# Kernel tuning notes

Hardware: AMD Instinct MI355X
Metric: run time of the kernel (lower is better)

## Reference

```python
import jax, jax.numpy as jnp
import numpy as np

N_E = 8192
DIM = 256
BETA = 0.25


def _l2norm(x, eps=1e-12):
    # matches F.normalize(p=2, dim=-1): x / max(||x||, eps)
    n = jnp.sqrt(jnp.sum(x * x, axis=-1, keepdims=True))
    return x / jnp.maximum(n, eps)


def setup_inputs() -> dict:
    key = jax.random.key(0)
    k1, k2 = jax.random.split(key)
    z = jax.random.normal(k1, (8, 1024, DIM), dtype=jnp.float32)
    embedding_weight = jax.random.normal(k2, (N_E, DIM), dtype=jnp.float32)
    return {"z": z, "embedding_weight": embedding_weight}


def reference(z, embedding_weight):
    z = _l2norm(z)                                   # [B,S,D]
    zf = z.reshape(-1, DIM)                          # [N,D]
    embed_norm = _l2norm(embedding_weight)           # [n_e,D]
    # d = ||z||^2 + ||e||^2 - 2 z.e  -> [N, n_e]
    d = (jnp.sum(zf * zf, axis=1, keepdims=True)
         + jnp.sum(embed_norm * embed_norm, axis=1)
         - 2.0 * jnp.einsum('bd,nd->bn', zf, embed_norm))
    encoding_indices = jnp.argmin(d, axis=1).reshape(z.shape[:-1])  # [B,S]
    z_q = embedding_weight[encoding_indices]          # gather raw codes
    z_q = _l2norm(z_q)                                # [B,S,D]
    loss = (BETA * jnp.mean((jax.lax.stop_gradient(z_q) - z) ** 2)
            + jnp.mean((z_q - jax.lax.stop_gradient(z)) ** 2))
    z_q = z + jax.lax.stop_gradient(z_q - z)          # straight-through
    return z_q, loss, encoding_indices
```

## Files before the change

kernel.cpp:

```cpp
#include <hip/hip_runtime.h>
#include <hip/hip_fp16.h>
#include <cfloat>
#include <math.h>

#define DIM    256
#define N_TOK  8192
#define N_E    8192
#define NSEG   1024
#define MARGIN 0.012f

typedef __attribute__((ext_vector_type(8))) short bf16x8;
typedef __attribute__((ext_vector_type(4))) float f32x4;
typedef __attribute__((ext_vector_type(8))) unsigned short ushort8;

__device__ __forceinline__ unsigned short f2bf(float f) {
    unsigned u = __float_as_uint(f);
    unsigned r = u + 0x7fff + ((u >> 16) & 1);
    return (unsigned short)(r >> 16);
}
__device__ __forceinline__ unsigned fkey(float f) {
    unsigned u = __float_as_uint(f);
    return (u & 0x80000000u) ? ~u : (u | 0x80000000u);
}
__device__ __forceinline__ unsigned short f2h(float f) {
    const __half h = __float2half(f);
    return *(const unsigned short*)&h;
}
__device__ __forceinline__ float h2f(unsigned short u) {
    __half_raw r; r.x = u;
    return __half2float((__half)r);
}

__global__ __launch_bounds__(256) void l2norm_all(const float* __restrict__ z,
                                                  const float* __restrict__ emb,
                                                  float* __restrict__ zn,
                                                  unsigned short* __restrict__ zb,
                                                  float* __restrict__ en,
                                                  unsigned short* __restrict__ esw,
                                                  float* __restrict__ e2) {
    const int lane = threadIdx.x & 63;
    const bool isE = blockIdx.x < (N_E / 4);
    const int row = (isE ? blockIdx.x : blockIdx.x - N_E / 4) * 4 + (threadIdx.x >> 6);
    const float* in = isE ? emb : z;
    float* out = isE ? en : zn;
    const float4 v = *(const float4*)(in + row * DIM + lane * 4);
    float s = v.x * v.x + v.y * v.y + v.z * v.z + v.w * v.w;
#pragma unroll
    for (int off = 1; off < 64; off <<= 1) s += __shfl_xor(s, off, 64);
    const float inv = 1.0f / fmaxf(sqrtf(s), 1e-12f);
    const float4 o = make_float4(v.x * inv, v.y * inv, v.z * inv, v.w * inv);
    *(float4*)(out + row * DIM + lane * 4) = o;
    ushort4 ob; ob.x = f2bf(o.x); ob.y = f2bf(o.y); ob.z = f2bf(o.z); ob.w = f2bf(o.w);
    if (isE) {
        const int k0 = lane * 4;
        const size_t sidx = ((size_t)((row >> 4) * 8 + (k0 >> 5)) * 64
                             + ((k0 >> 3) & 3) * 16 + (row & 15)) * 8 + (k0 & 7);
        *(ushort4*)(esw + sidx) = ob;
        float q = o.x * o.x + o.y * o.y + o.z * o.z + o.w * o.w;
#pragma unroll
        for (int off = 1; off < 64; off <<= 1) q += __shfl_xor(q, off, 64);
        if (lane == 0) e2[row] = q;
    } else {
        *(ushort4*)(zb + row * DIM + lane * 4) = ob;
    }
}

__global__ __launch_bounds__(256, 3) void mfma_dist(const unsigned short* __restrict__ zb,
                                                    const unsigned short* __restrict__ esw,
                                                    const float* __restrict__ e2,
                                                    unsigned short* __restrict__ segMh) {
    __shared__ __align__(16) unsigned short As[128][32];
    __shared__ float sm[16][128];

    const int tid  = threadIdx.x;
    const int lane = tid & 63;
    const int wave = tid >> 6;
    const int wm = wave & 1, wn = wave >> 1;
    const int row0 = (blockIdx.x & 63) * 128;
    const int col0 = (blockIdx.x >> 6) * 128;
    const int fr = lane & 15, q = lane >> 4;

    f32x4 acc[4][4];
#pragma unroll
    for (int ci = 0; ci < 4; ci++)
#pragma unroll
        for (int zi = 0; zi < 4; zi++) acc[ci][zi] = (f32x4){0.f, 0.f, 0.f, 0.f};

    const int aBase = (col0 >> 4) + wn * 4;
    auto la = [&](int i, int kc) {
        return *(const bf16x8*)(esw + (size_t)(aBase + i) * 4096 + kc * 512 + lane * 8);
    };
    const int srow  = lane >> 2;
    const int skoff = (lane & 3) * 8;
    const unsigned short* gZ = zb + (row0 + wave * 32 + srow) * DIM + skoff;

    bf16x8 ca[2][4];
#pragma unroll
    for (int i = 0; i < 4; i++) ca[0][i] = la(i, 0);

#pragma unroll
    for (int kc = 0; kc < 8; kc++) {
        const int cur = kc & 1, nxt = cur ^ 1;
        if (kc < 7) {
#pragma unroll
            for (int i = 0; i < 4; i++) ca[nxt][i] = la(i, kc + 1);
        }
        __syncthreads();
#pragma unroll
        for (int j = 0; j < 2; j++) {
            __builtin_amdgcn_global_load_lds(
                (const __attribute__((address_space(1))) unsigned int*)(gZ + j * 16 * DIM + kc * 32),
                (__attribute__((address_space(3))) unsigned int*)&As[wave * 32 + j * 16][0],
                16, 0, 0);
        }
        __syncthreads();
        bf16x8 zfr[4];
#pragma unroll
        for (int i = 0; i < 4; i++) zfr[i] = *(const bf16x8*)&As[wm * 64 + i * 16 + fr][q * 8];
#pragma unroll
        for (int ci = 0; ci < 4; ci++)
#pragma unroll
            for (int zi = 0; zi < 4; zi++)
                acc[ci][zi] = __builtin_amdgcn_mfma_f32_16x16x32_bf16(ca[cur][ci], zfr[zi], acc[ci][zi], 0, 0, 0);
    }

    float4 e2q[4];
#pragma unroll
    for (int ci = 0; ci < 4; ci++)
        e2q[ci] = *(const float4*)&e2[col0 + wn * 64 + ci * 16 + q * 4];
#pragma unroll
    for (int ci = 0; ci < 4; ci++) {
#pragma unroll
        for (int zi = 0; zi < 4; zi++) {
            const float t0 = fmaf(-2.0f, acc[ci][zi][0], e2q[ci].x);
            const float t1 = fmaf(-2.0f, acc[ci][zi][1], e2q[ci].y);
            const float t2 = fmaf(-2.0f, acc[ci][zi][2], e2q[ci].z);
            const float t3 = fmaf(-2.0f, acc[ci][zi][3], e2q[ci].w);
            float mm = fminf(fminf(t0, t1), fminf(t2, t3));
            mm = fminf(mm, __shfl_xor(mm, 16, 64));
            if (q == 0) sm[wn * 8 + ci * 2 + 0][wm * 64 + zi * 16 + fr] = mm;
            if (q == 2) sm[wn * 8 + ci * 2 + 1][wm * 64 + zi * 16 + fr] = mm;
        }
    }
    __syncthreads();
    {
        const int rl = tid & 127, part = tid >> 7;
        ushort8 o8;
#pragma unroll
        for (int j = 0; j < 8; j++) o8[j] = f2h(sm[part * 8 + j][rl]);
        *(ushort8*)&segMh[(size_t)(row0 + rl) * NSEG + (col0 >> 3) + part * 8] = o8;
    }
}

__global__ __launch_bounds__(256) void select_rescore(const unsigned short* __restrict__ segMh,
                                                      const float* __restrict__ en,
                                                      const float* __restrict__ e2,
                                                      float* zq,
                                                      float* out_base,
                                                      float* __restrict__ pl) {
    const int lane = threadIdx.x & 63;
    const int row  = (blockIdx.x << 2) + (threadIdx.x >> 6);
    const unsigned short* ph = segMh + (size_t)row * NSEG + lane * 16;
    const ushort8 u0 = *(const ushort8*)ph;
    const ushort8 u1 = *(const ushort8*)(ph + 8);
    float vv[16];
#pragma unroll
    for (int j = 0; j < 8; j++) { vv[j] = h2f(u0[j]); vv[8 + j] = h2f(u1[j]); }
    float m = vv[0];
#pragma unroll
    for (int j = 1; j < 16; j++) m = fminf(m, vv[j]);
#pragma unroll
    for (int off = 1; off < 64; off <<= 1) m = fminf(m, __shfl_xor(m, off, 64));
    const float thr = m + MARGIN;

    const int q = lane >> 4, f = lane & 15;
    const float4* zp = (const float4*)(zq + (size_t)row * DIM);
    float4 z4[4];
#pragma unroll
    for (int j = 0; j < 4; j++) z4[j] = zp[j * 16 + f];

    unsigned long long pk = ~0ull;
#pragma unroll
    for (int j = 0; j < 16; j++) {
        unsigned long long bal = __ballot(vv[j] <= thr);
        while (bal) {
            const int l = __ffsll(bal) - 1;
            bal &= bal - 1;
            const int seg = l * 16 + j;
#pragma unroll
            for (int g = 0; g < 2; g++) {
                const int col = seg * 8 + g * 4 + q;
                const float4* ep = (const float4*)(en + (size_t)col * DIM);
                float s = 0.f;
#pragma unroll
                for (int jj = 0; jj < 4; jj++) {
                    const float4 ev = ep[jj * 16 + f];
                    s = fmaf(z4[jj].x, ev.x, s); s = fmaf(z4[jj].y, ev.y, s);
                    s = fmaf(z4[jj].z, ev.z, s); s = fmaf(z4[jj].w, ev.w, s);
                }
#pragma unroll
                for (int off = 1; off < 16; off <<= 1) s += __shfl_xor(s, off, 64);
                const float d = fmaf(-2.0f, s, e2[col]);
                const unsigned long long key =
                    ((unsigned long long)fkey(d) << 32) | (unsigned)col;
                if (key < pk) pk = key;
            }
        }
    }
#pragma unroll
    for (int off = 16; off < 64; off <<= 1) {
        const unsigned long long o = __shfl_xor(pk, off, 64);
        if (o < pk) pk = o;
    }
    const int i = (int)(pk & 0xffffffffu);

    const float4 qv = *(const float4*)(en + (size_t)i * DIM + lane * 4);
    const float4 zv = *(const float4*)(zq + (size_t)row * DIM + lane * 4);
    const float dx = qv.x - zv.x, dy = qv.y - zv.y, dz = qv.z - zv.z, dw = qv.w - zv.w;
    float s = dx * dx + dy * dy + dz * dz + dw * dw;
    *(float4*)(zq + (size_t)row * DIM + lane * 4) = qv;
#pragma unroll
    for (int off = 1; off < 64; off <<= 1) s += __shfl_xor(s, off, 64);
    if (lane == 0) {
        pl[row] = s;
        out_base[N_TOK * DIM + 1 + row] = (float)i;
    }
}

__global__ __launch_bounds__(1024) void finalize_loss(const float* __restrict__ pl,
                                                      float* __restrict__ out) {
    __shared__ float sw[16];
    const int t = threadIdx.x;
    float s = 0.f;
#pragma unroll
    for (int j = 0; j < 8; j++) s += pl[t + j * 1024];
#pragma unroll
    for (int off = 1; off < 64; off <<= 1) s += __shfl_xor(s, off, 64);
    if ((t & 63) == 0) sw[t >> 6] = s;
    __syncthreads();
    if (t < 16) {
        float v = sw[t];
#pragma unroll
        for (int off = 1; off < 16; off <<= 1) v += __shfl_xor(v, off, 64);
        if (t == 0) out[N_TOK * DIM] = v * (1.25f / 2097152.0f);
    }
}

extern "C" void kernel_launch(void* const* d_in, const int* in_sizes, int n_in,
                              void* d_out, int out_size, void* d_ws, size_t ws_size,
                              hipStream_t stream) {
    const float* z   = (const float*)d_in[0];
    const float* emb = (const float*)d_in[1];
    float* out = (float*)d_out;
    char* ws = (char*)d_ws;

    float*          en    = (float*)(ws);
    unsigned short* esw   = (unsigned short*)(ws + 8388608);
    unsigned short* zb    = (unsigned short*)(ws + 12582912);
    float*          e2    = (float*)(ws + 16777216);
    unsigned short* segMh = (unsigned short*)(ws + 16809984);
    float*          pl    = (float*)(ws + 33587200);

    l2norm_all<<<(N_E + N_TOK) / 4, 256, 0, stream>>>(z, emb, out, zb, en, esw, e2);
    mfma_dist<<<64 * 64, 256, 0, stream>>>(zb, esw, e2, segMh);
    select_rescore<<<N_TOK / 4, 256, 0, stream>>>(segMh, en, e2, out, out, pl);
    finalize_loss<<<1, 1024, 0, stream>>>(pl, out);
}
```

Before: 138.9 us.

## Load full-K z tile into swizzled LDS once and deepen codebook prefetch

The z tile for the whole K=256 extent is now staged into LDS in a single batch of global_load_lds calls, replacing the per-chunk load plus two barriers per K step. The normalize kernel writes z in an XOR-swizzled layout so that LDS fragment reads avoid bank conflicts. Codebook fragments are prefetched two chunks ahead into a larger register array, and the epilogue scratch reuses the same LDS buffer. In exchange, LDS grows to 64KB per block, occupancy is lowered to 2 blocks per SM, and register pressure rises.

```diff
diff --git a/kernel.cpp b/kernel.cpp
--- a/kernel.cpp
+++ b/kernel.cpp
@@ -51,8 +51,8 @@
     const float4 o = make_float4(v.x * inv, v.y * inv, v.z * inv, v.w * inv);
     *(float4*)(out + row * DIM + lane * 4) = o;
     ushort4 ob; ob.x = f2bf(o.x); ob.y = f2bf(o.y); ob.z = f2bf(o.z); ob.w = f2bf(o.w);
+    const int k0 = lane * 4;
     if (isE) {
-        const int k0 = lane * 4;
         const size_t sidx = ((size_t)((row >> 4) * 8 + (k0 >> 5)) * 64
                              + ((k0 >> 3) & 3) * 16 + (row & 15)) * 8 + (k0 & 7);
         *(ushort4*)(esw + sidx) = ob;
@@ -61,16 +61,18 @@
         for (int off = 1; off < 64; off <<= 1) q += __shfl_xor(q, off, 64);
         if (lane == 0) e2[row] = q;
     } else {
-        *(ushort4*)(zb + row * DIM + lane * 4) = ob;
-    }
-}
-
-__global__ __launch_bounds__(256, 3) void mfma_dist(const unsigned short* __restrict__ zb,
+        const int c = k0 >> 3;
+        const int p = c ^ (row & 31);
+        *(ushort4*)(zb + (size_t)row * DIM + p * 8 + (k0 & 7)) = ob;
+    }
+}
+
+__global__ __launch_bounds__(256, 2) void mfma_dist(const unsigned short* __restrict__ zb,
                                                     const unsigned short* __restrict__ esw,
                                                     const float* __restrict__ e2,
                                                     unsigned short* __restrict__ segMh) {
-    __shared__ __align__(16) unsigned short As[128][32];
-    __shared__ float sm[16][128];
+    __shared__ __align__(16) unsigned short As[128 * 256];
+    float* sm = reinterpret_cast<float*>(As);
 
     const int tid  = threadIdx.x;
     const int lane = tid & 63;
@@ -90,44 +92,49 @@
     auto la = [&](int i, int kc) {
         return *(const bf16x8*)(esw + (size_t)(aBase + i) * 4096 + kc * 512 + lane * 8);
     };
-    const int srow  = lane >> 2;
-    const int skoff = (lane & 3) * 8;
-    const unsigned short* gZ = zb + (row0 + wave * 32 + srow) * DIM + skoff;
-
-    bf16x8 ca[2][4];
-#pragma unroll
-    for (int i = 0; i < 4; i++) ca[0][i] = la(i, 0);
+    auto lz = [&](int i, int kc) {
+        const int r = wm * 64 + i * 16 + fr;
+        const int c = kc * 4 + q;
+        return *(const bf16x8*)&As[r * 256 + ((c ^ (r & 31)) * 8)];
+    };
+
+    bf16x8 ca[8][4];
+#pragma unroll
+    for (int i = 0; i < 4; i++) { ca[0][i] = la(i, 0); ca[1][i] = la(i, 1); }
+
+    {
+        const unsigned short* gZ = zb + (size_t)(row0 + wave * 32) * DIM;
+#pragma unroll
+        for (int j = 0; j < 16; j++) {
+            __builtin_amdgcn_global_load_lds(
+                (const __attribute__((address_space(1))) unsigned int*)(gZ + j * 2 * DIM + lane * 8),
+                (__attribute__((address_space(3))) unsigned int*)&As[(wave * 32 + j * 2) * 256],
+                16, 0, 0);
+        }
+    }
+    __syncthreads();
 
 #pragma unroll
     for (int kc = 0; kc < 8; kc++) {
-        const int cur = kc & 1, nxt = cur ^ 1;
-        if (kc < 7) {
-#pragma unroll
-            for (int i = 0; i < 4; i++) ca[nxt][i] = la(i, kc + 1);
-        }
-        __syncthreads();
-#pragma unroll
-        for (int j = 0; j < 2; j++) {
-            __builtin_amdgcn_global_load_lds(
-                (const __attribute__((address_space(1))) unsigned int*)(gZ + j * 16 * DIM + kc * 32),
-                (__attribute__((address_space(3))) unsigned int*)&As[wave * 32 + j * 16][0],
-                16, 0, 0);
-        }
-        __syncthreads();
+        if (kc + 2 < 8) {
+#pragma unroll
+            for (int i = 0; i < 4; i++) ca[kc + 2][i] = la(i, kc + 2);
+        }
         bf16x8 zfr[4];
 #pragma unroll
-        for (int i = 0; i < 4; i++) zfr[i] = *(const bf16x8*)&As[wm * 64 + i * 16 + fr][q * 8];
+        for (int i = 0; i < 4; i++) zfr[i] = lz(i, kc);
 #pragma unroll
         for (int ci = 0; ci < 4; ci++)
 #pragma unroll
             for (int zi = 0; zi < 4; zi++)
-                acc[ci][zi] = __builtin_amdgcn_mfma_f32_16x16x32_bf16(ca[cur][ci], zfr[zi], acc[ci][zi], 0, 0, 0);
+                acc[ci][zi] = __builtin_amdgcn_mfma_f32_16x16x32_bf16(ca[kc][ci], zfr[zi], acc[ci][zi], 0, 0, 0);
     }
 
     float4 e2q[4];
 #pragma unroll
     for (int ci = 0; ci < 4; ci++)
         e2q[ci] = *(const float4*)&e2[col0 + wn * 64 + ci * 16 + q * 4];
+    __syncthreads();
 #pragma unroll
     for (int ci = 0; ci < 4; ci++) {
 #pragma unroll
@@ -138,8 +145,8 @@
             const float t3 = fmaf(-2.0f, acc[ci][zi][3], e2q[ci].w);
             float mm = fminf(fminf(t0, t1), fminf(t2, t3));
             mm = fminf(mm, __shfl_xor(mm, 16, 64));
-            if (q == 0) sm[wn * 8 + ci * 2 + 0][wm * 64 + zi * 16 + fr] = mm;
-            if (q == 2) sm[wn * 8 + ci * 2 + 1][wm * 64 + zi * 16 + fr] = mm;
+            if (q == 0) sm[(wn * 8 + ci * 2 + 0) * 128 + wm * 64 + zi * 16 + fr] = mm;
+            if (q == 2) sm[(wn * 8 + ci * 2 + 1) * 128 + wm * 64 + zi * 16 + fr] = mm;
         }
     }
     __syncthreads();
@@ -147,7 +154,7 @@
         const int rl = tid & 127, part = tid >> 7;
         ushort8 o8;
 #pragma unroll
-        for (int j = 0; j < 8; j++) o8[j] = f2h(sm[part * 8 + j][rl]);
+        for (int j = 0; j < 8; j++) o8[j] = f2h(sm[(part * 8 + j) * 128 + rl]);
         *(ushort8*)&segMh[(size_t)(row0 + rl) * NSEG + (col0 >> 3) + part * 8] = o8;
     }
 }
```

New measurement: 158.2 us. 1.14x slower.
